# Performance work log

Measured on AMD Instinct MI355X. Metric: run time of the kernel, lower is better.

The kernel has to match this reference:

```python
import jax, jax.numpy as jnp
import numpy as np

N_ATOMS = 200000
N_EDGES = 800000
ATOM_FDIM = 133
HIDDEN = 256
NUM_MOLS = 8000
ALPHA = 0.2  # LeakyReLU slope


def setup_inputs() -> dict:
    key = jax.random.key(0)
    ks = jax.random.split(key, 10)
    f_atoms = jax.random.normal(ks[0], (N_ATOMS, ATOM_FDIM), dtype=jnp.float32)
    edge_index = jax.random.randint(ks[1], (2, N_EDGES), 0, N_ATOMS, dtype=jnp.int64)
    mol_ids = jnp.sort(jax.random.randint(ks[2], (N_ATOMS,), 0, NUM_MOLS, dtype=jnp.int64))
    s0 = 1.0 / np.sqrt(ATOM_FDIM)
    sh = 1.0 / np.sqrt(HIDDEN)
    sa = 1.0 / np.sqrt(2 * HIDDEN)
    W0 = jax.random.normal(ks[3], (ATOM_FDIM, HIDDEN), dtype=jnp.float32) * s0
    a0 = jax.random.normal(ks[4], (2 * HIDDEN,), dtype=jnp.float32) * sa
    W1 = jax.random.normal(ks[5], (HIDDEN, HIDDEN), dtype=jnp.float32) * sh
    a1 = jax.random.normal(ks[6], (2 * HIDDEN,), dtype=jnp.float32) * sa
    W2 = jax.random.normal(ks[7], (HIDDEN, HIDDEN), dtype=jnp.float32) * sh
    a2 = jax.random.normal(ks[8], (2 * HIDDEN,), dtype=jnp.float32) * sa
    return {"f_atoms": f_atoms, "edge_index": edge_index, "mol_ids": mol_ids,
            "W0": W0, "a0": a0, "W1": W1, "a1": a1, "W2": W2, "a2": a2}


def _gat_layer(x, W, a, src, tgt, residual):
    # x: [N, Fin], W: [Fin, H], a: [2H]
    h = x @ W                              # [N, H]
    H = h.shape[1]
    a_s, a_t = a[:H], a[H:]
    # e = leakyrelu([h_src || h_tgt] @ a), computed without materializing the concat
    e = jax.nn.leaky_relu(h[src] @ a_s + h[tgt] @ a_t, negative_slope=ALPHA)  # [E]
    att = jnp.exp(e)
    denom = jax.ops.segment_sum(att, tgt, num_segments=x.shape[0])            # [N]
    att_n = att / (denom[tgt] + 1e-8)
    # weighted scatter-aggregate (dropout is a no-op in eval mode)
    h_prime = jax.ops.segment_sum(h[src] * att_n[:, None], tgt, num_segments=x.shape[0])
    if residual:
        h_prime = h_prime + x
    return jax.nn.elu(h_prime)


def reference(f_atoms, edge_index, mol_ids, W0, a0, W1, a1, W2, a2):
    src, tgt = edge_index[0], edge_index[1]
    x = _gat_layer(f_atoms, W0, a0, src, tgt, residual=False)
    x = _gat_layer(x, W1, a1, src, tgt, residual=True)
    x = _gat_layer(x, W2, a2, src, tgt, residual=True)
    # per-molecule mean pooling (a_scope loop -> segment mean)
    sums = jax.ops.segment_sum(x, mol_ids, num_segments=NUM_MOLS)            # [M, H]
    counts = jax.ops.segment_sum(jnp.ones((x.shape[0],), x.dtype), mol_ids, num_segments=NUM_MOLS)
    return jnp.where(counts[:, None] > 0, sums / jnp.maximum(counts[:, None], 1.0), 0.0)
```

## Files before the change

### kernel.cpp

```cpp
#include <hip/hip_runtime.h>

#define N_ATOMS 200000
#define N_EDGES 800000
#define FDIM    133
#define HID     256
#define NMOLS   8000
#define CAP     32

typedef unsigned short bf16_t;
typedef __attribute__((ext_vector_type(4))) float f32x4;
typedef __attribute__((ext_vector_type(8))) short bf16x8;

__device__ inline float bf2f(bf16_t u) {
    union { unsigned int i; float f; } v; v.i = ((unsigned int)u) << 16; return v.f;
}
__device__ inline bf16_t f2bf(float f) {
    union { float f; unsigned int i; } v; v.f = f;
    return (bf16_t)((v.i + 0x7fffu + ((v.i >> 16) & 1u)) >> 16);
}
__device__ inline float4 ld4(const bf16_t* p) {
    ushort4 u = *(const ushort4*)p;
    return make_float4(bf2f(u.x), bf2f(u.y), bf2f(u.z), bf2f(u.w));
}

__device__ inline void gload_lds16(const void* g, void* l) {
    __builtin_amdgcn_global_load_lds((const __attribute__((address_space(1))) unsigned int*)g,
                                     (__attribute__((address_space(3))) unsigned int*)l,
                                     16, 0, 0);
}

__global__ __launch_bounds__(256) void build_adj(const int* __restrict__ ei,
                                                 int* __restrict__ cnt,
                                                 int* __restrict__ lst) {
    int e = blockIdx.x * 256 + threadIdx.x;
    if (e >= N_EDGES) return;
    int s = ei[e];
    int t = ei[N_EDGES + e];
    int p = atomicAdd(&cnt[t], 1);
    if (p < CAP) lst[t * CAP + p] = s;
}

__global__ __launch_bounds__(256) void transpose_w(const float* __restrict__ W,
                                                   bf16_t* __restrict__ Wt,
                                                   int K, int Kpad) {
    int idx = blockIdx.x * 256 + threadIdx.x;
    if (idx >= HID * Kpad) return;
    int n = idx / Kpad, k = idx - n * Kpad;
    Wt[idx] = (k < K) ? f2bf(W[k * HID + n]) : (bf16_t)0;
}

template <bool A_FP32, int KSTEPS, int LDA, int KP>
__global__ __launch_bounds__(1024, 4) void gemm_mfma(const void* __restrict__ Av,
                                                     const bf16_t* __restrict__ Wt,
                                                     bf16_t* __restrict__ H,
                                                     const float* __restrict__ avec,
                                                     float* __restrict__ ss_o,
                                                     float* __restrict__ st_o) {
    __shared__ bf16_t As[2][256][32];
    __shared__ bf16_t Bs[2][256][32];
    __shared__ float  red[2][256][4];
    const int tid  = threadIdx.x;
    const int lane = tid & 63;
    const int w    = tid >> 6;
    const int wr   = w >> 2;
    const int wc   = w & 3;
    const int fr   = lane & 15;
    const int kg   = lane >> 4;
    const int row0 = blockIdx.x * 256;

    const int sra  = tid >> 2;
    const int ska  = (tid & 3) * 8;
    int sgrow = row0 + sra; if (sgrow >= N_ATOMS) sgrow = N_ATOMS - 1;

    float sreg[8];

#define ISSUE(ks_, buf_) do {                                                          \
    const int k0_ = (ks_) * 32;                                                        \
    if constexpr (A_FP32) {                                                            \
        _Pragma("unroll")                                                              \
        for (int j = 0; j < 8; ++j) {                                                  \
            int gk = k0_ + ska + j;                                                    \
            sreg[j] = (gk < LDA) ? ((const float*)Av)[(long long)sgrow * LDA + gk] : 0.f; \
        }                                                                              \
    } else {                                                                           \
        gload_lds16((const bf16_t*)Av + (long long)sgrow * LDA + k0_ + ska,            \
                    (char*)&As[buf_][0][0] + w * 1024);                                \
    }                                                                                  \
    gload_lds16(Wt + (long long)(tid >> 2) * KP + k0_ + ska,                           \
                (char*)&Bs[buf_][0][0] + w * 1024);                                    \
} while (0)

#define COMMIT(buf_) do {                                                              \
    if constexpr (A_FP32) {                                                            \
        short v_[8];                                                                   \
        _Pragma("unroll")                                                              \
        for (int j = 0; j < 8; ++j) v_[j] = (short)f2bf(sreg[j]);                      \
        *(bf16x8*)&As[buf_][sra][ska] = *(bf16x8*)&v_[0];                              \
    }                                                                                  \
} while (0)

#define READ_FRAGS(buf_, af_, bf_) do {                                                \
    const int koff_ = kg * 8;                                                          \
    _Pragma("unroll")                                                                  \
    for (int i = 0; i < 4; ++i)                                                        \
        af_[i] = *(const bf16x8*)&As[buf_][wr * 64 + i * 16 + fr][koff_];              \
    _Pragma("unroll")                                                                  \
    for (int jn = 0; jn < 4; ++jn)                                                     \
        bf_[jn] = *(const bf16x8*)&Bs[buf_][wc * 64 + jn * 16 + fr][koff_];            \
} while (0)

#define DO_MFMA(af_, bf_) do {                                                         \
    _Pragma("unroll")                                                                  \
    for (int i = 0; i < 4; ++i)                                                        \
        _Pragma("unroll")                                                              \
        for (int jn = 0; jn < 4; ++jn)                                                 \
            acc[i][jn] = __builtin_amdgcn_mfma_f32_16x16x32_bf16(af_[i], bf_[jn], acc[i][jn], 0, 0, 0); \
} while (0)

    f32x4 acc[4][4] = {};

    if constexpr (A_FP32) {
        ISSUE(0, 0);
        COMMIT(0);
        __syncthreads();
        int buf = 0;
        for (int ks = 0; ks < KSTEPS; ++ks) {
            if (ks + 1 < KSTEPS) ISSUE(ks + 1, buf ^ 1);
            bf16x8 af[4], bfr[4];
            READ_FRAGS(buf, af, bfr);
            DO_MFMA(af, bfr);
            if (ks + 1 < KSTEPS) COMMIT(buf ^ 1);
            __syncthreads();
            buf ^= 1;
        }
    } else {
        ISSUE(0, 0);
        int buf = 0;
        for (int ks = 0; ks < KSTEPS; ++ks) {
            if (ks + 1 < KSTEPS) {
                ISSUE(ks + 1, buf ^ 1);
                asm volatile("s_waitcnt vmcnt(2)" ::: "memory");
            } else {
                asm volatile("s_waitcnt vmcnt(0)" ::: "memory");
            }
            __builtin_amdgcn_s_barrier();

            bf16x8 af[4], bfr[4];
            READ_FRAGS(buf, af, bfr);
            asm volatile("s_waitcnt lgkmcnt(0)" ::: "memory");
            __builtin_amdgcn_sched_barrier(0);
            __builtin_amdgcn_s_barrier();

            DO_MFMA(af, bfr);
            buf ^= 1;
        }
    }
#undef ISSUE
#undef COMMIT
#undef READ_FRAGS
#undef DO_MFMA

    float as_v[4], at_v[4];
    #pragma unroll
    for (int jn = 0; jn < 4; ++jn) {
        int c = wc * 64 + jn * 16 + fr;
        as_v[jn] = avec[c];
        at_v[jn] = avec[HID + c];
    }
    #pragma unroll
    for (int i = 0; i < 4; ++i) {
        #pragma unroll
        for (int rr = 0; rr < 4; ++rr) {
            int row_l = wr * 64 + i * 16 + kg * 4 + rr;
            int r = row0 + row_l;
            float ps = 0.f, pt = 0.f;
            #pragma unroll
            for (int jn = 0; jn < 4; ++jn) {
                float h = acc[i][jn][rr];
                ps += h * as_v[jn];
                pt += h * at_v[jn];
                if (r < N_ATOMS)
                    H[(long long)r * HID + (wc * 64 + jn * 16 + fr)] = f2bf(h);
            }
            #pragma unroll
            for (int o = 1; o < 16; o <<= 1) {
                ps += __shfl_xor(ps, o);
                pt += __shfl_xor(pt, o);
            }
            if (fr == 0) {
                red[0][row_l][wc] = ps;
                red[1][row_l][wc] = pt;
            }
        }
    }
    __syncthreads();
    if (tid < 256) {
        int r = row0 + tid;
        if (r < N_ATOMS) {
            ss_o[r] = (red[0][tid][0] + red[0][tid][1]) + (red[0][tid][2] + red[0][tid][3]);
            st_o[r] = (red[1][tid][0] + red[1][tid][1]) + (red[1][tid][2] + red[1][tid][3]);
        }
    }
}

__global__ __launch_bounds__(256) void aggregate(const bf16_t* __restrict__ H,
                                                 const float* __restrict__ ss,
                                                 const float* __restrict__ st,
                                                 const int* __restrict__ cnt,
                                                 const int* __restrict__ lst,
                                                 bf16_t* __restrict__ X,
                                                 int residual) {
    const int tid  = threadIdx.x;
    const int lane = tid & 63;
    const int wv   = (blockIdx.x * 256 + tid) >> 6;
    const int half = lane >> 5;
    const int sub  = lane & 31;
    const int t    = 2 * wv + half;

    int n = cnt[t]; if (n > CAP) n = CAP;

    const float stt = st[t];
    const unsigned rowoff = (unsigned)t * (HID * 2);
    const unsigned loff   = (unsigned)sub * 16;
    const unsigned lbase  = (unsigned)t * (CAP * 4);

    float acc[8] = {0.f, 0.f, 0.f, 0.f, 0.f, 0.f, 0.f, 0.f};
    float denom = 0.f;

    for (int i0 = 0; i0 < n; i0 += 4) {
        int4 s4 = *(const int4*)((const char*)lst + (lbase + (unsigned)i0 * 4));
        int s0 = s4.x;
        int s1 = (i0 + 1 < n) ? s4.y : s4.x;
        int s2 = (i0 + 2 < n) ? s4.z : s4.x;
        int s3 = (i0 + 3 < n) ? s4.w : s4.x;

        float v0 = ss[s0], v1 = ss[s1], v2 = ss[s2], v3 = ss[s3];

        bf16x8 r0 = *(const bf16x8*)((const char*)H + ((unsigned)s0 * 512u + loff));
        bf16x8 r1 = *(const bf16x8*)((const char*)H + ((unsigned)s1 * 512u + loff));
        bf16x8 r2 = *(const bf16x8*)((const char*)H + ((unsigned)s2 * 512u + loff));
        bf16x8 r3 = *(const bf16x8*)((const char*)H + ((unsigned)s3 * 512u + loff));

        float e0 = v0 + stt; e0 = e0 > 0.f ? e0 : 0.2f * e0;
        float e1 = v1 + stt; e1 = e1 > 0.f ? e1 : 0.2f * e1;
        float e2 = v2 + stt; e2 = e2 > 0.f ? e2 : 0.2f * e2;
        float e3 = v3 + stt; e3 = e3 > 0.f ? e3 : 0.2f * e3;

        float w0 = __expf(e0);
        float w1 = (i0 + 1 < n) ? __expf(e1) : 0.f;
        float w2 = (i0 + 2 < n) ? __expf(e2) : 0.f;
        float w3 = (i0 + 3 < n) ? __expf(e3) : 0.f;

        denom += (w0 + w1) + (w2 + w3);
        #pragma unroll
        for (int e = 0; e < 8; ++e) {
            acc[e] += w0 * bf2f((bf16_t)r0[e]) + w1 * bf2f((bf16_t)r1[e])
                    + w2 * bf2f((bf16_t)r2[e]) + w3 * bf2f((bf16_t)r3[e]);
        }
    }

    const float inv = 1.f / (denom + 1e-8f);
    float r[8];
    #pragma unroll
    for (int e = 0; e < 8; ++e) r[e] = acc[e] * inv;

    if (residual) {
        bf16x8 xv = *(const bf16x8*)((const char*)X + (rowoff + loff));
        #pragma unroll
        for (int e = 0; e < 8; ++e) r[e] += bf2f((bf16_t)xv[e]);
    }

    bf16x8 o;
    #pragma unroll
    for (int e = 0; e < 8; ++e) {
        float x = r[e];
        x = x > 0.f ? x : (__expf(x) - 1.f);
        o[e] = (short)f2bf(x);
    }
    *(bf16x8*)((char*)X + (rowoff + loff)) = o;
}

__device__ inline int lower_bound_i(const int* a, int n, int v) {
    int lo = 0, hi = n;
    while (lo < hi) { int mid = (lo + hi) >> 1; if (a[mid] < v) lo = mid + 1; else hi = mid; }
    return lo;
}

__global__ __launch_bounds__(64) void pool_kernel(const bf16_t* __restrict__ X,
                                                  const int* __restrict__ mol,
                                                  float* __restrict__ out) {
    int m = blockIdx.x;
    int lane = threadIdx.x;
    int lo = lower_bound_i(mol, N_ATOMS, m);
    int hi = lower_bound_i(mol, N_ATOMS, m + 1);
    float ax = 0.f, ay = 0.f, az = 0.f, aw = 0.f;
    for (int i = lo; i < hi; ++i) {
        float4 v = ld4(&X[(long long)i * HID + lane * 4]);
        ax += v.x; ay += v.y; az += v.z; aw += v.w;
    }
    float c = (float)(hi - lo);
    float4 r = make_float4(0.f, 0.f, 0.f, 0.f);
    if (c > 0.f) {
        float inv = 1.f / c;
        r = make_float4(ax * inv, ay * inv, az * inv, aw * inv);
    }
    *(float4*)&out[(long long)m * HID + lane * 4] = r;
}

extern "C" void kernel_launch(void* const* d_in, const int* in_sizes, int n_in,
                              void* d_out, int out_size, void* d_ws, size_t ws_size,
                              hipStream_t stream) {
    const float* f_atoms = (const float*)d_in[0];
    const int*   ei      = (const int*)d_in[1];
    const int*   mol     = (const int*)d_in[2];
    const float* W0      = (const float*)d_in[3];
    const float* a0      = (const float*)d_in[4];
    const float* W1      = (const float*)d_in[5];
    const float* a1      = (const float*)d_in[6];
    const float* W2      = (const float*)d_in[7];
    const float* a2      = (const float*)d_in[8];
    float* out = (float*)d_out;

    char* ws = (char*)d_ws;
    size_t off = 0;
    bf16_t* X  = (bf16_t*)(ws + off); off += (size_t)N_ATOMS * HID * 2;
    bf16_t* Hb = (bf16_t*)(ws + off); off += (size_t)N_ATOMS * HID * 2;
    float* ss  = (float*)(ws + off);  off += (size_t)N_ATOMS * 4;
    float* st  = (float*)(ws + off);  off += (size_t)N_ATOMS * 4;
    int* cnt   = (int*)(ws + off);    off += (size_t)N_ATOMS * 4;
    int* lst   = (int*)(ws + off);    off += (size_t)N_ATOMS * CAP * 4;
    if (ws_size < off) return;

    bf16_t* Wt = (bf16_t*)d_out;

    hipMemsetAsync(cnt, 0, (size_t)N_ATOMS * 4, stream);
    build_adj<<<(N_EDGES + 255) / 256, 256, 0, stream>>>(ei, cnt, lst);

    const int gemm_blocks = (N_ATOMS + 255) / 256;
    const int agg_blocks  = N_ATOMS / 8;

    transpose_w<<<(HID * 160 + 255) / 256, 256, 0, stream>>>(W0, Wt, FDIM, 160);
    gemm_mfma<true, 5, FDIM, 160><<<gemm_blocks, 1024, 0, stream>>>(f_atoms, Wt, Hb, a0, ss, st);
    aggregate<<<agg_blocks, 256, 0, stream>>>(Hb, ss, st, cnt, lst, X, 0);

    transpose_w<<<(HID * HID + 255) / 256, 256, 0, stream>>>(W1, Wt, HID, HID);
    gemm_mfma<false, 8, HID, HID><<<gemm_blocks, 1024, 0, stream>>>(X, Wt, Hb, a1, ss, st);
    aggregate<<<agg_blocks, 256, 0, stream>>>(Hb, ss, st, cnt, lst, X, 1);

    transpose_w<<<(HID * HID + 255) / 256, 256, 0, stream>>>(W2, Wt, HID, HID);
    gemm_mfma<false, 8, HID, HID><<<gemm_blocks, 1024, 0, stream>>>(X, Wt, Hb, a2, ss, st);
    aggregate<<<agg_blocks, 256, 0, stream>>>(Hb, ss, st, cnt, lst, X, 1);

    pool_kernel<<<NMOLS, 64, 0, stream>>>(X, mol, out);
}
```

Baseline: 566.7 us.

## Split GEMM into 64x128 tiles over a 2D grid with partial attention dots

The projection GEMM moves from 256-row, 1024-thread blocks covering all 256 output columns to 64x128 tiles with 256 threads on a 2D grid. This gives more, smaller blocks and better occupancy across CUs. Because each block now covers only half the columns, the attention source/target dot products are written as two partials into scratch space in the output buffer. A new combine_dots kernel then adds them. The cost is re-reading the A rows twice, extra kernel launches and extra partial-sum traffic, and bounds checks are dropped because 200000 is a multiple of 64.

```diff
diff --git a/kernel.cpp b/kernel.cpp
--- a/kernel.cpp
+++ b/kernel.cpp
@@ -50,27 +50,28 @@
 }
 
 template <bool A_FP32, int KSTEPS, int LDA, int KP>
-__global__ __launch_bounds__(1024, 4) void gemm_mfma(const void* __restrict__ Av,
-                                                     const bf16_t* __restrict__ Wt,
-                                                     bf16_t* __restrict__ H,
-                                                     const float* __restrict__ avec,
-                                                     float* __restrict__ ss_o,
-                                                     float* __restrict__ st_o) {
-    __shared__ bf16_t As[2][256][32];
-    __shared__ bf16_t Bs[2][256][32];
-    __shared__ float  red[2][256][4];
+__global__ __launch_bounds__(256, 5) void gemm_mfma(const void* __restrict__ Av,
+                                                    const bf16_t* __restrict__ Wt,
+                                                    bf16_t* __restrict__ H,
+                                                    const float* __restrict__ avec,
+                                                    float* __restrict__ ssp,
+                                                    float* __restrict__ stp) {
+    __shared__ bf16_t As[2][64][32];
+    __shared__ bf16_t Bs[2][128][32];
+    __shared__ float  red[2][64][2];
     const int tid  = threadIdx.x;
     const int lane = tid & 63;
     const int w    = tid >> 6;
-    const int wr   = w >> 2;
-    const int wc   = w & 3;
+    const int wr   = w >> 1;
+    const int wc   = w & 1;
     const int fr   = lane & 15;
     const int kg   = lane >> 4;
-    const int row0 = blockIdx.x * 256;
+    const int row0 = blockIdx.x * 64;
+    const int n0   = blockIdx.y * 128;
 
     const int sra  = tid >> 2;
     const int ska  = (tid & 3) * 8;
-    int sgrow = row0 + sra; if (sgrow >= N_ATOMS) sgrow = N_ATOMS - 1;
+    const int sgrow = row0 + sra;
 
     float sreg[8];
 
@@ -86,8 +87,10 @@
         gload_lds16((const bf16_t*)Av + (long long)sgrow * LDA + k0_ + ska,            \
                     (char*)&As[buf_][0][0] + w * 1024);                                \
     }                                                                                  \
-    gload_lds16(Wt + (long long)(tid >> 2) * KP + k0_ + ska,                           \
+    gload_lds16(Wt + (long long)(n0 + (tid >> 2)) * KP + k0_ + ska,                    \
                 (char*)&Bs[buf_][0][0] + w * 1024);                                    \
+    gload_lds16(Wt + (long long)(n0 + 64 + (tid >> 2)) * KP + k0_ + ska,               \
+                (char*)&Bs[buf_][0][0] + 4096 + w * 1024);                             \
 } while (0)
 
 #define COMMIT(buf_) do {                                                              \
@@ -102,8 +105,8 @@
 #define READ_FRAGS(buf_, af_, bf_) do {                                                \
     const int koff_ = kg * 8;                                                          \
     _Pragma("unroll")                                                                  \
-    for (int i = 0; i < 4; ++i)                                                        \
-        af_[i] = *(const bf16x8*)&As[buf_][wr * 64 + i * 16 + fr][koff_];              \
+    for (int i = 0; i < 2; ++i)                                                        \
+        af_[i] = *(const bf16x8*)&As[buf_][wr * 32 + i * 16 + fr][koff_];              \
     _Pragma("unroll")                                                                  \
     for (int jn = 0; jn < 4; ++jn)                                                     \
         bf_[jn] = *(const bf16x8*)&Bs[buf_][wc * 64 + jn * 16 + fr][koff_];            \
@@ -111,13 +114,13 @@
 
 #define DO_MFMA(af_, bf_) do {                                                         \
     _Pragma("unroll")                                                                  \
-    for (int i = 0; i < 4; ++i)                                                        \
+    for (int i = 0; i < 2; ++i)                                                        \
         _Pragma("unroll")                                                              \
         for (int jn = 0; jn < 4; ++jn)                                                 \
             acc[i][jn] = __builtin_amdgcn_mfma_f32_16x16x32_bf16(af_[i], bf_[jn], acc[i][jn], 0, 0, 0); \
 } while (0)
 
-    f32x4 acc[4][4] = {};
+    f32x4 acc[2][4] = {};
 
     if constexpr (A_FP32) {
         ISSUE(0, 0);
@@ -126,7 +129,7 @@
         int buf = 0;
         for (int ks = 0; ks < KSTEPS; ++ks) {
             if (ks + 1 < KSTEPS) ISSUE(ks + 1, buf ^ 1);
-            bf16x8 af[4], bfr[4];
+            bf16x8 af[2], bfr[4];
             READ_FRAGS(buf, af, bfr);
             DO_MFMA(af, bfr);
             if (ks + 1 < KSTEPS) COMMIT(buf ^ 1);
@@ -139,13 +142,13 @@
         for (int ks = 0; ks < KSTEPS; ++ks) {
             if (ks + 1 < KSTEPS) {
                 ISSUE(ks + 1, buf ^ 1);
-                asm volatile("s_waitcnt vmcnt(2)" ::: "memory");
+                asm volatile("s_waitcnt vmcnt(3)" ::: "memory");
             } else {
                 asm volatile("s_waitcnt vmcnt(0)" ::: "memory");
             }
             __builtin_amdgcn_s_barrier();
 
-            bf16x8 af[4], bfr[4];
+            bf16x8 af[2], bfr[4];
             READ_FRAGS(buf, af, bfr);
             asm volatile("s_waitcnt lgkmcnt(0)" ::: "memory");
             __builtin_amdgcn_sched_barrier(0);
@@ -163,15 +166,15 @@
     float as_v[4], at_v[4];
     #pragma unroll
     for (int jn = 0; jn < 4; ++jn) {
-        int c = wc * 64 + jn * 16 + fr;
+        int c = n0 + wc * 64 + jn * 16 + fr;
         as_v[jn] = avec[c];
         at_v[jn] = avec[HID + c];
     }
     #pragma unroll
-    for (int i = 0; i < 4; ++i) {
+    for (int i = 0; i < 2; ++i) {
         #pragma unroll
         for (int rr = 0; rr < 4; ++rr) {
-            int row_l = wr * 64 + i * 16 + kg * 4 + rr;
+            int row_l = wr * 32 + i * 16 + kg * 4 + rr;
             int r = row0 + row_l;
             float ps = 0.f, pt = 0.f;
             #pragma unroll
@@ -179,8 +182,7 @@
                 float h = acc[i][jn][rr];
                 ps += h * as_v[jn];
                 pt += h * at_v[jn];
-                if (r < N_ATOMS)
-                    H[(long long)r * HID + (wc * 64 + jn * 16 + fr)] = f2bf(h);
+                H[(long long)r * HID + (n0 + wc * 64 + jn * 16 + fr)] = f2bf(h);
             }
             #pragma unroll
             for (int o = 1; o < 16; o <<= 1) {
@@ -194,13 +196,22 @@
         }
     }
     __syncthreads();
-    if (tid < 256) {
+    if (tid < 64) {
         int r = row0 + tid;
-        if (r < N_ATOMS) {
-            ss_o[r] = (red[0][tid][0] + red[0][tid][1]) + (red[0][tid][2] + red[0][tid][3]);
-            st_o[r] = (red[1][tid][0] + red[1][tid][1]) + (red[1][tid][2] + red[1][tid][3]);
-        }
-    }
+        long long slot = (long long)blockIdx.y * N_ATOMS + r;
+        ssp[slot] = red[0][tid][0] + red[0][tid][1];
+        stp[slot] = red[1][tid][0] + red[1][tid][1];
+    }
+}
+
+__global__ __launch_bounds__(256) void combine_dots(const float* __restrict__ ssp,
+                                                    const float* __restrict__ stp,
+                                                    float* __restrict__ ss,
+                                                    float* __restrict__ st) {
+    int i = blockIdx.x * 256 + threadIdx.x;
+    if (i >= N_ATOMS) return;
+    ss[i] = ssp[i] + ssp[N_ATOMS + i];
+    st[i] = stp[i] + stp[N_ATOMS + i];
 }
 
 __global__ __launch_bounds__(256) void aggregate(const bf16_t* __restrict__ H,
@@ -331,24 +342,31 @@
     int* lst   = (int*)(ws + off);    off += (size_t)N_ATOMS * CAP * 4;
     if (ws_size < off) return;
 
-    bf16_t* Wt = (bf16_t*)d_out;
+    char* ob = (char*)d_out;
+    bf16_t* Wt  = (bf16_t*)ob;
+    float*  ssp = (float*)(ob + 131072);
+    float*  stp = (float*)(ob + 131072 + 1600000);
 
     hipMemsetAsync(cnt, 0, (size_t)N_ATOMS * 4, stream);
     build_adj<<<(N_EDGES + 255) / 256, 256, 0, stream>>>(ei, cnt, lst);
 
-    const int gemm_blocks = (N_ATOMS + 255) / 256;
-    const int agg_blocks  = N_ATOMS / 8;
+    const dim3 gemm_grid(N_ATOMS / 64, 2);
+    const int  agg_blocks = N_ATOMS / 8;
+    const int  cmb_blocks = (N_ATOMS + 255) / 256;
 
     transpose_w<<<(HID * 160 + 255) / 256, 256, 0, stream>>>(W0, Wt, FDIM, 160);
-    gemm_mfma<true, 5, FDIM, 160><<<gemm_blocks, 1024, 0, stream>>>(f_atoms, Wt, Hb, a0, ss, st);
+    gemm_mfma<true, 5, FDIM, 160><<<gemm_grid, 256, 0, stream>>>(f_atoms, Wt, Hb, a0, ssp, stp);
+    combine_dots<<<cmb_blocks, 256, 0, stream>>>(ssp, stp, ss, st);
     aggregate<<<agg_blocks, 256, 0, stream>>>(Hb, ss, st, cnt, lst, X, 0);
 
     transpose_w<<<(HID * HID + 255) / 256, 256, 0, stream>>>(W1, Wt, HID, HID);
-    gemm_mfma<false, 8, HID, HID><<<gemm_blocks, 1024, 0, stream>>>(X, Wt, Hb, a1, ss, st);
+    gemm_mfma<false, 8, HID, HID><<<gemm_grid, 256, 0, stream>>>(X, Wt, Hb, a1, ssp, stp);
+    combine_dots<<<cmb_blocks, 256, 0, stream>>>(ssp, stp, ss, st);
     aggregate<<<agg_blocks, 256, 0, stream>>>(Hb, ss, st, cnt, lst, X, 1);
 
     transpose_w<<<(HID * HID + 255) / 256, 256, 0, stream>>>(W2, Wt, HID, HID);
-    gemm_mfma<false, 8, HID, HID><<<gemm_blocks, 1024, 0, stream>>>(X, Wt, Hb, a2, ss, st);
+    gemm_mfma<false, 8, HID, HID><<<gemm_grid, 256, 0, stream>>>(X, Wt, Hb, a2, ssp, stp);
+    combine_dots<<<cmb_blocks, 256, 0, stream>>>(ssp, stp, ss, st);
     aggregate<<<agg_blocks, 256, 0, stream>>>(Hb, ss, st, cnt, lst, X, 1);
 
     pool_kernel<<<NMOLS, 64, 0, stream>>>(X, mol, out);
```

Measured after the change: 570.9 us. Within noise of the previous version (+0.7%).
